# Kernel tuning notes

Hardware: AMD Instinct MI355X
Metric: run time of the kernel (lower is better)

## Reference

```python
import jax, jax.numpy as jnp
import numpy as np

HEAD_SIZE = 64


def setup_inputs() -> dict:
    key = jax.random.key(0)
    k1, k2, k3, k4 = jax.random.split(key, 4)
    B, T, C, H = 8, 2048, 1024, HEAD_SIZE
    return {
        "idx": jax.random.normal(k1, (B, T, C), dtype=jnp.float32),
        "Wk": jax.random.normal(k2, (C, H), dtype=jnp.float32) * (C ** -0.5),
        "Wq": jax.random.normal(k3, (C, H), dtype=jnp.float32) * (C ** -0.5),
        "Wv": jax.random.normal(k4, (C, H), dtype=jnp.float32) * (C ** -0.5),
    }


def reference(idx, Wk, Wq, Wv):
    # idx: [B, T, C]; Wk/Wq/Wv: [C, H]
    B, T, C = idx.shape
    H = Wk.shape[1]
    k = idx @ Wk  # [B, T, H]
    q = idx @ Wq  # [B, T, H]
    v = idx @ Wv  # [B, T, H]
    # Faithful to source: wei = k @ q^T (note: k first, as written in the torch code)
    wei = jnp.einsum("bth,bsh->bts", k, q) * (H ** -0.5)  # [B, T, T]
    causal = jnp.tril(jnp.ones((T, T), dtype=bool))
    wei = jnp.where(causal, wei, -jnp.inf)
    wei = jax.nn.softmax(wei, axis=-1)
    # Dropout(0.5) treated as eval-mode identity (deterministic reference)
    out = jnp.einsum("bts,bsh->bth", wei, v)  # [B, T, H]
    return out
```

## Files before the change

kernel.cpp:

```cpp
#include <hip/hip_runtime.h>

#define B_ 8
#define T_ 2048
#define C_ 1024
#define H_ 64
#define BT_ (B_ * T_)

typedef float f32x4 __attribute__((ext_vector_type(4)));
typedef unsigned short u16x4 __attribute__((ext_vector_type(4)));
typedef unsigned short u16x8 __attribute__((ext_vector_type(8)));
typedef __bf16 bf16x8 __attribute__((ext_vector_type(8)));

static __device__ __forceinline__ unsigned short f2bf(float f) {
    unsigned int u = __builtin_bit_cast(unsigned int, f);
    u = (u + 0x7FFFu + ((u >> 16) & 1u)) >> 16;
    return (unsigned short)u;
}

static __device__ __forceinline__ f32x4 mfma16(u16x8 a, u16x8 b, f32x4 c) {
    return __builtin_amdgcn_mfma_f32_16x16x32_bf16(
        __builtin_bit_cast(bf16x8, a), __builtin_bit_cast(bf16x8, b), c, 0, 0, 0);
}

static __device__ __forceinline__ void cvtpk4(float a0, float a1, float a2, float a3,
                                              unsigned& d0, unsigned& d1) {
    asm("v_cvt_pk_bf16_f32 %0, %1, %2" : "=v"(d0) : "v"(a0), "v"(a1));
    asm("v_cvt_pk_bf16_f32 %0, %1, %2" : "=v"(d1) : "v"(a2), "v"(a3));
}

static __device__ __forceinline__ void gload_lds16(const void* g, void* l) {
    auto gp = (const __attribute__((address_space(1))) char*)(
        reinterpret_cast<uintptr_t>(g));
    auto lp = (__attribute__((address_space(3))) char*)(
        reinterpret_cast<uintptr_t>(l));
    __builtin_amdgcn_global_load_lds(gp, lp, 16, 0, 0);
}

static __device__ __forceinline__ int Pof(int j) {
    return 5 - (j >= 2 ? 1 : 0) - (j >= 6 ? 1 : 0);
}
static __device__ __forceinline__ int offsof(int j) {
    return (j < 2) ? 5 * j : (j < 6 ? 4 * j + 2 : 3 * j + 8);
}

__global__ __launch_bounds__(256) void wprep(const float* __restrict__ Wk,
                                             const float* __restrict__ Wq,
                                             const float* __restrict__ Wv,
                                             unsigned short* __restrict__ wt) {
    __shared__ float tile[64][65];
    const int arr = blockIdx.x >> 4, ct = blockIdx.x & 15;
    const float* W = (arr == 0) ? Wk : ((arr == 1) ? Wq : Wv);
    const int tid = threadIdx.x;
    {
        int c = tid >> 2, seg = (tid & 3) << 4;
        const float* src = W + (size_t)(ct * 64 + c) * 64 + seg;
#pragma unroll
        for (int j = 0; j < 16; j += 4) {
            f32x4 v4 = *(const f32x4*)(src + j);
            tile[c][seg + j + 0] = v4[0];
            tile[c][seg + j + 1] = v4[1];
            tile[c][seg + j + 2] = v4[2];
            tile[c][seg + j + 3] = v4[3];
        }
    }
    __syncthreads();
    {
        int h = tid >> 2, cs = (tid & 3) << 4;
        unsigned short* dst = wt + (size_t)(arr * 64 + h) * 1024 + ct * 64 + cs;
#pragma unroll
        for (int j = 0; j < 16; ++j) dst[j] = f2bf(tile[cs + j][h]);
    }
}

__global__ __launch_bounds__(512, 4) void proj_gemm(const float* __restrict__ idx,
                                                    const unsigned short* __restrict__ wt,
                                                    unsigned short* __restrict__ kw,
                                                    unsigned short* __restrict__ qw,
                                                    unsigned short* __restrict__ vtw) {
    __shared__ unsigned short As[2][32 * 64];
    __shared__ unsigned short Bs[2][192 * 64];
    const int tid = threadIdx.x;
    const int lane = tid & 63, w = tid >> 6;
    const int g = lane >> 4, l15 = lane & 15;
    const int m0 = blockIdx.x * 32;
    const int arow = tid >> 4, aseg = tid & 15;

    f32x4 acc[3] = {};
    f32x4 areg[2];

    auto sloadA = [&](int set, int k0) {
        areg[set] = *(const f32x4*)(idx + (size_t)(m0 + arow) * 1024 + k0 + aseg * 4);
    };
    auto swriteA = [&](int set, int buf) {
        unsigned d0, d1;
        cvtpk4(areg[set][0], areg[set][1], areg[set][2], areg[set][3], d0, d1);
        int au = aseg >> 1, ah = aseg & 1;
        uint2 pk; pk.x = d0; pk.y = d1;
        *(uint2*)&As[buf][arow * 64 + ((au ^ (arow & 7)) * 8) + ah * 4] = pk;
    };
    auto stageB = [&](int k0, int buf) {
#pragma unroll
        for (int i = 0; i < 3; ++i) {
            int slot0 = i * 512 + w * 64;
            int n = i * 64 + w * 8 + (lane >> 3);
            int us = (lane & 7) ^ (lane >> 3);
            gload_lds16(wt + (size_t)n * 1024 + k0 + us * 8,
                        &Bs[buf][slot0 * 8]);
        }
    };

    stageB(0, 0);
    sloadA(0, 0);
    sloadA(1, 64);
    swriteA(0, 0);
    __syncthreads();

    for (int kt = 0; kt < 16; ++kt) {
        const int cur = kt & 1;
        if (kt < 15) stageB((kt + 1) * 64, cur ^ 1);
        if (kt < 14) sloadA(cur, (kt + 2) * 64);
#pragma unroll
        for (int ks = 0; ks < 2; ++ks) {
            u16x8 a = *(const u16x8*)&As[cur][((w & 1) * 16 + l15) * 64 +
                                              (((ks * 4 + g) ^ (l15 & 7)) * 8)];
#pragma unroll
            for (int nf = 0; nf < 3; ++nf) {
                int n = (w >> 1) * 48 + nf * 16 + l15;
                u16x8 b = *(const u16x8*)&Bs[cur][n * 64 + (((ks * 4 + g) ^ (n & 7)) * 8)];
                acc[nf] = mfma16(a, b, acc[nf]);
            }
        }
        if (kt < 15) swriteA(cur ^ 1, cur ^ 1);
        __syncthreads();
    }

#pragma unroll
    for (int nf = 0; nf < 3; ++nf) {
        int nb = (w >> 1) * 3 + nf;
        int arr = nb >> 2;
        int nloc = ((nb & 3) << 4) + l15;
        f32x4 ac = acc[nf];
        int row = m0 + (w & 1) * 16 + g * 4;
        if (arr == 2) {
            u16x4 pk = {f2bf(ac[0]), f2bf(ac[1]), f2bf(ac[2]), f2bf(ac[3])};
            *(u16x4*)&vtw[(size_t)nloc * BT_ + row] = pk;
        } else {
            unsigned short* dst = arr ? qw : kw;
            dst[(size_t)(row + 0) * 64 + nloc] = f2bf(ac[0]);
            dst[(size_t)(row + 1) * 64 + nloc] = f2bf(ac[1]);
            dst[(size_t)(row + 2) * 64 + nloc] = f2bf(ac[2]);
            dst[(size_t)(row + 3) * 64 + nloc] = f2bf(ac[3]);
        }
    }
}

__global__ __launch_bounds__(512, 2) void attn_part(const unsigned short* __restrict__ kw,
                                                    const unsigned short* __restrict__ qw,
                                                    const unsigned short* __restrict__ vtw,
                                                    float* __restrict__ Opart,
                                                    float* __restrict__ lpart) {
    __shared__ unsigned short q_s[2][64 * 64];
    __shared__ unsigned short v_s[2][64 * 64];
    __shared__ unsigned short p_s[8 * 32 * 64];
    const int tid = threadIdx.x;
    const int w = tid >> 6, lane = tid & 63;
    const int g = lane >> 4, l15 = lane & 15;
    const int bid = blockIdx.x;
    const int b = bid & 7;
    const int rem = bid >> 3;
    const int j = (rem < 10) ? (rem / 5) : (rem < 26 ? (rem - 2) >> 2 : (rem - 8) / 3);
    const int P = Pof(j);
    const int part = rem - offsof(j);
    const size_t base = (size_t)b * T_;
    const int tA0 = 128 * j + 16 * w;
    const int tB0 = 128 * (15 - j) + 16 * w;
    const int nS = 2 * (16 - j);
    unsigned short* p_my = p_s + w * 2048;
    const float SCL = 0.125f * 1.44269504f;
    const float MOFF = 16.0f;

    u16x8 kf[2][2];
#pragma unroll
    for (int tf = 0; tf < 2; ++tf) {
        const unsigned short* kr = kw + (size_t)(base + (tf ? tB0 : tA0) + l15) * 64;
        kf[tf][0] = *(const u16x8*)(kr + g * 8);
        kf[tf][1] = *(const u16x8*)(kr + 32 + g * 8);
    }

    f32x4 o[4][2] = {};
    float l_lane[2] = {0.f, 0.f};

    auto stageQV = [&](int st, int buf) {
        int s0 = st << 6;
        int r = w * 8 + (lane >> 3);
        int us = (lane & 7) ^ (lane >> 3);
        gload_lds16(qw + (size_t)(base + s0 + r) * 64 + us * 8,
                    &q_s[buf][w * 512]);
        gload_lds16(vtw + (size_t)r * BT_ + base + s0 + us * 8,
                    &v_s[buf][w * 512]);
    };

    stageQV(part, 0);
    __syncthreads();

    int i = 0;
    for (int st = part; st < nS; st += P, ++i) {
        const int s0 = st << 6;
        const int buf = i & 1;
        const bool more = (st + P < nS);
        if (more) stageQV(st + P, buf ^ 1);
        const bool dA = (s0 <= tA0 + 15);
        const bool dB = (s0 <= tB0 + 15);

        u16x8 a[2][4];
#pragma unroll
        for (int ks = 0; ks < 2; ++ks)
#pragma unroll
            for (int sf = 0; sf < 4; ++sf)
                a[ks][sf] = *(const u16x8*)&q_s[buf][(sf * 16 + l15) * 64 +
                                                     (((ks * 4 + g) ^ (l15 & 7)) * 8)];

        f32x4 s_[4][2] = {};
        __builtin_amdgcn_s_setprio(1);
        if (dB) {
#pragma unroll
            for (int ks = 0; ks < 2; ++ks)
#pragma unroll
                for (int sf = 0; sf < 4; ++sf)
                    s_[sf][1] = mfma16(a[ks][sf], kf[1][ks], s_[sf][1]);
        }
        if (dA) {
#pragma unroll
            for (int ks = 0; ks < 2; ++ks)
#pragma unroll
                for (int sf = 0; sf < 4; ++sf)
                    s_[sf][0] = mfma16(a[ks][sf], kf[0][ks], s_[sf][0]);
        }
        __builtin_amdgcn_s_setprio(0);

#pragma unroll
        for (int tf_ = 1; tf_ >= 0; --tf_) {
            if (tf_ ? !dB : !dA) continue;
            const int tbase_ = tf_ ? tB0 : tA0;
            float pv[4][4];
#pragma unroll
            for (int sf = 0; sf < 4; ++sf)
#pragma unroll
                for (int r = 0; r < 4; ++r)
                    pv[sf][r] = exp2f(fmaf(s_[sf][tf_][r], SCL, -MOFF));
            if (s0 + 63 > tbase_) {
                const int t_ = tbase_ + l15;
#pragma unroll
                for (int sf = 0; sf < 4; ++sf)
#pragma unroll
                    for (int r = 0; r < 4; ++r) {
                        int sg = s0 + sf * 16 + g * 4 + r;
                        if (sg > t_) pv[sf][r] = 0.f;
                    }
            }
            float lacc = 0.f;
#pragma unroll
            for (int sf = 0; sf < 4; ++sf)
                lacc += (pv[sf][0] + pv[sf][1]) + (pv[sf][2] + pv[sf][3]);
            l_lane[tf_] += lacc;
            const int trow = tf_ * 16 + l15;
#pragma unroll
            for (int sf = 0; sf < 4; ++sf) {
                unsigned r0, r1;
                cvtpk4(pv[sf][0], pv[sf][1], pv[sf][2], pv[sf][3], r0, r1);
                int u16i = (sf * 2 + (g >> 1)) ^ (l15 & 7);
                uint2 pk; pk.x = r0; pk.y = r1;
                *(uint2*)&p_my[trow * 64 + u16i * 8 + (g & 1) * 4] = pk;
            }
        }

        u16x8 vf[2][4];
#pragma unroll
        for (int ks = 0; ks < 2; ++ks)
#pragma unroll
            for (int mf = 0; mf < 4; ++mf)
                vf[ks][mf] = *(const u16x8*)&v_s[buf][(mf * 16 + l15) * 64 +
                                                      (((ks * 4 + g) ^ (l15 & 7)) * 8)];
        __builtin_amdgcn_s_setprio(1);
#pragma unroll
        for (int ks = 0; ks < 2; ++ks) {
            if (dB) {
                u16x8 bp1 = *(const u16x8*)&p_my[(16 + l15) * 64 +
                                                 (((ks * 4 + g) ^ (l15 & 7)) * 8)];
#pragma unroll
                for (int mf = 0; mf < 4; ++mf)
                    o[mf][1] = mfma16(vf[ks][mf], bp1, o[mf][1]);
            }
            if (dA) {
                u16x8 bp0 = *(const u16x8*)&p_my[l15 * 64 +
                                                 (((ks * 4 + g) ^ (l15 & 7)) * 8)];
#pragma unroll
                for (int mf = 0; mf < 4; ++mf)
                    o[mf][0] = mfma16(vf[ks][mf], bp0, o[mf][0]);
            }
        }
        __builtin_amdgcn_s_setprio(0);

        __syncthreads();
    }

#pragma unroll
    for (int tf = 0; tf < 2; ++tf) {
        float ls = l_lane[tf];
        ls += __shfl_xor(ls, 16);
        ls += __shfl_xor(ls, 32);
        int rl = tf * 128 + w * 16 + l15;
        if (g == 0) lpart[(size_t)bid * 256 + rl] = ls;
#pragma unroll
        for (int mf = 0; mf < 4; ++mf)
            *(f32x4*)&Opart[(size_t)bid * 16384 + (size_t)rl * 64 + mf * 16 + g * 4] = o[mf][tf];
    }
}

__global__ __launch_bounds__(256) void attn_comb(const float* __restrict__ Opart,
                                                 const float* __restrict__ lpart,
                                                 float* __restrict__ out) {
    int gt = blockIdx.x * 256 + threadIdx.x;
    int row = gt >> 4;
    int h0 = (gt & 15) << 2;
    int b = row >> 11, t = row & 2047;
    int ti = t >> 7, rit = t & 127;
    int j = (ti < 8) ? ti : (15 - ti);
    int tf = (ti < 8) ? 0 : 1;
    int rl = tf * 128 + rit;
    int P = Pof(j), offs = offsof(j);
    f32x4 acc = {};
    float L = 0.f;
    for (int p = 0; p < P; ++p) {
        int pb = b + 8 * (offs + p);
        acc += *(const f32x4*)&Opart[(size_t)pb * 16384 + (size_t)rl * 64 + h0];
        L += lpart[(size_t)pb * 256 + rl];
    }
    float inv = 1.f / L;
    *(f32x4*)&out[(size_t)row * 64 + h0] = acc * inv;
}

extern "C" void kernel_launch(void* const* d_in, const int* in_sizes, int n_in,
                              void* d_out, int out_size, void* d_ws, size_t ws_size,
                              hipStream_t stream) {
    const float* idx = (const float*)d_in[0];
    const float* Wk = (const float*)d_in[1];
    const float* Wq = (const float*)d_in[2];
    const float* Wv = (const float*)d_in[3];
    float* out = (float*)d_out;

    unsigned short* wt = (unsigned short*)d_ws;
    unsigned short* kw = wt + 192 * 1024;
    unsigned short* qw = kw + (size_t)BT_ * 64;
    unsigned short* vtw = qw + (size_t)BT_ * 64;
    float* Opart = (float*)((char*)d_ws + (8u << 20));
    float* lpart = Opart + (size_t)256 * 16384;

    wprep<<<48, 256, 0, stream>>>(Wk, Wq, Wv, wt);
    proj_gemm<<<512, 512, 0, stream>>>(idx, wt, kw, qw, vtw);
    attn_part<<<256, 512, 0, stream>>>(kw, qw, vtw, Opart, lpart);
    attn_comb<<<1024, 256, 0, stream>>>(Opart, lpart, out);
}
```

Measured before the change: 48.90 us.

## Double projection GEMM M-tile and store attention partials in bf16

```diff
diff --git a/kernel.cpp b/kernel.cpp
--- a/kernel.cpp
+++ b/kernel.cpp
@@ -26,6 +26,15 @@
                                               unsigned& d0, unsigned& d1) {
     asm("v_cvt_pk_bf16_f32 %0, %1, %2" : "=v"(d0) : "v"(a0), "v"(a1));
     asm("v_cvt_pk_bf16_f32 %0, %1, %2" : "=v"(d1) : "v"(a2), "v"(a3));
+}
+
+static __device__ __forceinline__ f32x4 bf4f(u16x4 v) {
+    f32x4 r;
+    r[0] = __builtin_bit_cast(float, (unsigned)v[0] << 16);
+    r[1] = __builtin_bit_cast(float, (unsigned)v[1] << 16);
+    r[2] = __builtin_bit_cast(float, (unsigned)v[2] << 16);
+    r[3] = __builtin_bit_cast(float, (unsigned)v[3] << 16);
+    return r;
 }
 
 static __device__ __forceinline__ void gload_lds16(const void* g, void* l) {
@@ -72,31 +81,34 @@
     }
 }
 
-__global__ __launch_bounds__(512, 4) void proj_gemm(const float* __restrict__ idx,
+__global__ __launch_bounds__(512, 2) void proj_gemm(const float* __restrict__ idx,
                                                     const unsigned short* __restrict__ wt,
                                                     unsigned short* __restrict__ kw,
                                                     unsigned short* __restrict__ qw,
                                                     unsigned short* __restrict__ vtw) {
-    __shared__ unsigned short As[2][32 * 64];
+    __shared__ unsigned short As[2][64 * 64];
     __shared__ unsigned short Bs[2][192 * 64];
     const int tid = threadIdx.x;
     const int lane = tid & 63, w = tid >> 6;
     const int g = lane >> 4, l15 = lane & 15;
-    const int m0 = blockIdx.x * 32;
-    const int arow = tid >> 4, aseg = tid & 15;
-
-    f32x4 acc[3] = {};
-    f32x4 areg[2];
+    const int m0 = blockIdx.x * 64;
+    const int ar = tid >> 3, as_ = tid & 7;
+
+    f32x4 acc[2][3] = {};
+    f32x4 areg[2][2];
 
     auto sloadA = [&](int set, int k0) {
-        areg[set] = *(const f32x4*)(idx + (size_t)(m0 + arow) * 1024 + k0 + aseg * 4);
+        const f32x4* src = (const f32x4*)(idx + (size_t)(m0 + ar) * 1024 + k0 +
+                                          ((as_ ^ (ar & 7)) * 8));
+        areg[set][0] = src[0];
+        areg[set][1] = src[1];
     };
     auto swriteA = [&](int set, int buf) {
-        unsigned d0, d1;
-        cvtpk4(areg[set][0], areg[set][1], areg[set][2], areg[set][3], d0, d1);
-        int au = aseg >> 1, ah = aseg & 1;
-        uint2 pk; pk.x = d0; pk.y = d1;
-        *(uint2*)&As[buf][arow * 64 + ((au ^ (arow & 7)) * 8) + ah * 4] = pk;
+        unsigned d0, d1, d2, d3;
+        cvtpk4(areg[set][0][0], areg[set][0][1], areg[set][0][2], areg[set][0][3], d0, d1);
+        cvtpk4(areg[set][1][0], areg[set][1][1], areg[set][1][2], areg[set][1][3], d2, d3);
+        uint4 pk; pk.x = d0; pk.y = d1; pk.z = d2; pk.w = d3;
+        *(uint4*)&As[buf][ar * 64 + as_ * 8] = pk;
     };
     auto stageB = [&](int k0, int buf) {
 #pragma unroll
@@ -121,13 +133,16 @@
         if (kt < 14) sloadA(cur, (kt + 2) * 64);
 #pragma unroll
         for (int ks = 0; ks < 2; ++ks) {
-            u16x8 a = *(const u16x8*)&As[cur][((w & 1) * 16 + l15) * 64 +
-                                              (((ks * 4 + g) ^ (l15 & 7)) * 8)];
+            u16x8 a0 = *(const u16x8*)&As[cur][((w & 1) * 16 + l15) * 64 +
+                                               (((ks * 4 + g) ^ (l15 & 7)) * 8)];
+            u16x8 a1 = *(const u16x8*)&As[cur][(32 + (w & 1) * 16 + l15) * 64 +
+                                               (((ks * 4 + g) ^ (l15 & 7)) * 8)];
 #pragma unroll
             for (int nf = 0; nf < 3; ++nf) {
                 int n = (w >> 1) * 48 + nf * 16 + l15;
                 u16x8 b = *(const u16x8*)&Bs[cur][n * 64 + (((ks * 4 + g) ^ (n & 7)) * 8)];
-                acc[nf] = mfma16(a, b, acc[nf]);
+                acc[0][nf] = mfma16(a0, b, acc[0][nf]);
+                acc[1][nf] = mfma16(a1, b, acc[1][nf]);
             }
         }
         if (kt < 15) swriteA(cur ^ 1, cur ^ 1);
@@ -139,17 +154,20 @@
         int nb = (w >> 1) * 3 + nf;
         int arr = nb >> 2;
         int nloc = ((nb & 3) << 4) + l15;
-        f32x4 ac = acc[nf];
-        int row = m0 + (w & 1) * 16 + g * 4;
-        if (arr == 2) {
-            u16x4 pk = {f2bf(ac[0]), f2bf(ac[1]), f2bf(ac[2]), f2bf(ac[3])};
-            *(u16x4*)&vtw[(size_t)nloc * BT_ + row] = pk;
-        } else {
-            unsigned short* dst = arr ? qw : kw;
-            dst[(size_t)(row + 0) * 64 + nloc] = f2bf(ac[0]);
-            dst[(size_t)(row + 1) * 64 + nloc] = f2bf(ac[1]);
-            dst[(size_t)(row + 2) * 64 + nloc] = f2bf(ac[2]);
-            dst[(size_t)(row + 3) * 64 + nloc] = f2bf(ac[3]);
+#pragma unroll
+        for (int mi = 0; mi < 2; ++mi) {
+            f32x4 ac = acc[mi][nf];
+            int row = m0 + mi * 32 + (w & 1) * 16 + g * 4;
+            if (arr == 2) {
+                u16x4 pk = {f2bf(ac[0]), f2bf(ac[1]), f2bf(ac[2]), f2bf(ac[3])};
+                *(u16x4*)&vtw[(size_t)nloc * BT_ + row] = pk;
+            } else {
+                unsigned short* dst = arr ? qw : kw;
+                dst[(size_t)(row + 0) * 64 + nloc] = f2bf(ac[0]);
+                dst[(size_t)(row + 1) * 64 + nloc] = f2bf(ac[1]);
+                dst[(size_t)(row + 2) * 64 + nloc] = f2bf(ac[2]);
+                dst[(size_t)(row + 3) * 64 + nloc] = f2bf(ac[3]);
+            }
         }
     }
 }
@@ -157,7 +175,7 @@
 __global__ __launch_bounds__(512, 2) void attn_part(const unsigned short* __restrict__ kw,
                                                     const unsigned short* __restrict__ qw,
                                                     const unsigned short* __restrict__ vtw,
-                                                    float* __restrict__ Opart,
+                                                    unsigned short* __restrict__ Opart,
                                                     float* __restrict__ lpart) {
     __shared__ unsigned short q_s[2][64 * 64];
     __shared__ unsigned short v_s[2][64 * 64];
@@ -312,12 +330,16 @@
         int rl = tf * 128 + w * 16 + l15;
         if (g == 0) lpart[(size_t)bid * 256 + rl] = ls;
 #pragma unroll
-        for (int mf = 0; mf < 4; ++mf)
-            *(f32x4*)&Opart[(size_t)bid * 16384 + (size_t)rl * 64 + mf * 16 + g * 4] = o[mf][tf];
-    }
-}
-
-__global__ __launch_bounds__(256) void attn_comb(const float* __restrict__ Opart,
+        for (int mf = 0; mf < 4; ++mf) {
+            unsigned r0, r1;
+            cvtpk4(o[mf][tf][0], o[mf][tf][1], o[mf][tf][2], o[mf][tf][3], r0, r1);
+            uint2 pk; pk.x = r0; pk.y = r1;
+            *(uint2*)&Opart[(size_t)bid * 16384 + (size_t)rl * 64 + mf * 16 + g * 4] = pk;
+        }
+    }
+}
+
+__global__ __launch_bounds__(256) void attn_comb(const unsigned short* __restrict__ Opart,
                                                  const float* __restrict__ lpart,
                                                  float* __restrict__ out) {
     int gt = blockIdx.x * 256 + threadIdx.x;
@@ -333,7 +355,8 @@
     float L = 0.f;
     for (int p = 0; p < P; ++p) {
         int pb = b + 8 * (offs + p);
-        acc += *(const f32x4*)&Opart[(size_t)pb * 16384 + (size_t)rl * 64 + h0];
+        u16x4 ov = *(const u16x4*)&Opart[(size_t)pb * 16384 + (size_t)rl * 64 + h0];
+        acc += bf4f(ov);
         L += lpart[(size_t)pb * 256 + rl];
     }
     float inv = 1.f / L;
@@ -353,11 +376,11 @@
     unsigned short* kw = wt + 192 * 1024;
     unsigned short* qw = kw + (size_t)BT_ * 64;
     unsigned short* vtw = qw + (size_t)BT_ * 64;
-    float* Opart = (float*)((char*)d_ws + (8u << 20));
-    float* lpart = Opart + (size_t)256 * 16384;
+    unsigned short* Opart = (unsigned short*)((char*)d_ws + (8u << 20));
+    float* lpart = (float*)((char*)d_ws + (18u << 20));
 
     wprep<<<48, 256, 0, stream>>>(Wk, Wq, Wv, wt);
-    proj_gemm<<<512, 512, 0, stream>>>(idx, wt, kw, qw, vtw);
+    proj_gemm<<<256, 512, 0, stream>>>(idx, wt, kw, qw, vtw);
     attn_part<<<256, 512, 0, stream>>>(kw, qw, vtw, Opart, lpart);
     attn_comb<<<1024, 256, 0, stream>>>(Opart, lpart, out);
 }
```

Measured after the change: 47.82 us (median of 2 runs). -2.2%, faster.
